# Kernel tuning notes

Measured on AMD Instinct MI355X. Metric: run time of the kernel, lower is better.

Reference implementation:

```python
import jax, jax.numpy as jnp
import numpy as np

NUM_TOKENS = 50000
TOKEN_DIM = 1024
HIDDEN = 2048
NUM_LABEL = 50000
T = 512
MAX_LEN = 50  # length-classifier has 50 classes -> max decode steps


def setup_inputs() -> dict:
    key = jax.random.key(0)
    ks = jax.random.split(key, 20)
    s = 0.02
    def nrm(k, shape):
        return jax.random.normal(k, shape, dtype=jnp.float32) * s
    return {
        "x": jax.random.randint(ks[0], (T,), 0, NUM_TOKENS),
        "E": nrm(ks[1], (NUM_TOKENS, TOKEN_DIM)),
        "L": nrm(ks[2], (NUM_LABEL, HIDDEN)),
        # forward encoder GRU (torch layout: W_ih [3H, in], W_hh [3H, H])
        "Wih_f": nrm(ks[3], (3 * HIDDEN, TOKEN_DIM)),
        "Whh_f": nrm(ks[4], (3 * HIDDEN, HIDDEN)),
        "bih_f": nrm(ks[5], (3 * HIDDEN,)),
        "bhh_f": nrm(ks[6], (3 * HIDDEN,)),
        # backward encoder GRU
        "Wih_b": nrm(ks[7], (3 * HIDDEN, TOKEN_DIM)),
        "Whh_b": nrm(ks[8], (3 * HIDDEN, HIDDEN)),
        "bih_b": nrm(ks[9], (3 * HIDDEN,)),
        "bhh_b": nrm(ks[10], (3 * HIDDEN,)),
        # middle / length linears
        "W_mid": nrm(ks[11], (HIDDEN, 2 * HIDDEN)),
        "b_mid": nrm(ks[12], (HIDDEN,)),
        "W_len": nrm(ks[13], (MAX_LEN, HIDDEN)),
        "b_len": nrm(ks[14], (MAX_LEN,)),
        # decoder GRU (input size 2H)
        "Wih_d": nrm(ks[15], (3 * HIDDEN, 2 * HIDDEN)),
        "Whh_d": nrm(ks[16], (3 * HIDDEN, HIDDEN)),
        "bih_d": nrm(ks[17], (3 * HIDDEN,)),
        "bhh_d": nrm(ks[18], (3 * HIDDEN,)),
        # final classifier (no bias)
        "W_last": nrm(ks[19], (NUM_LABEL, HIDDEN)),
    }


def _gru_final_hidden(emb, Wih, Whh, bih, bhh):
    """Run a single-layer GRU over emb [T, in] from h0=0; return final hidden [H]."""
    def step(h, x):
        gi = x @ Wih.T + bih          # [3H]
        gh = h @ Whh.T + bhh          # [3H]
        ir, iz, inn = jnp.split(gi, 3)
        hr, hz, hn = jnp.split(gh, 3)
        r = jax.nn.sigmoid(ir + hr)
        z = jax.nn.sigmoid(iz + hz)
        n = jnp.tanh(inn + r * hn)
        return (1.0 - z) * n + z * h, None
    h0 = jnp.zeros((Whh.shape[1],), emb.dtype)
    hT, _ = jax.lax.scan(step, h0, emb)
    return hT


def reference(x, E, L, Wih_f, Whh_f, bih_f, bhh_f, Wih_b, Whh_b, bih_b, bhh_b,
              W_mid, b_mid, W_len, b_len, Wih_d, Whh_d, bih_d, bhh_d, W_last):
    emb = E[x]  # [T, token_dim]
    hF = _gru_final_hidden(emb, Wih_f, Whh_f, bih_f, bhh_f)
    hB = _gru_final_hidden(emb[::-1], Wih_b, Whh_b, bih_b, bhh_b)
    sent = jnp.concatenate([hF, hB]) @ W_mid.T + b_mid   # [H]
    lscores = sent @ W_len.T + b_len                      # [50]

    # Decoder: original passes h as the GRU *input* with a fresh zero hidden
    # each step, so h-side gate preactivations reduce to bhh_d.
    hr_d, hz_d, hn_d = jnp.split(bhh_d, 3)

    def dec_step(carry, _):
        gi = carry @ Wih_d.T + bih_d          # carry: [2H]
        ir, iz, inn = jnp.split(gi, 3)
        r = jax.nn.sigmoid(ir + hr_d)
        z = jax.nn.sigmoid(iz + hz_d)
        n = jnp.tanh(inn + r * hn_d)
        h = (1.0 - z) * n                     # + z * 0 since h0 = 0
        scores = h @ W_last.T                 # [num_label]
        pred = jnp.argmax(scores)
        return jnp.concatenate([h, L[pred]]), (scores, pred)

    init = jnp.concatenate([jnp.zeros((HIDDEN,), sent.dtype), sent])
    _, (all_scores, preds) = jax.lax.scan(dec_step, init, None, length=MAX_LEN)
    # fixed MAX_LEN-step unroll; original stops at argmax(lscores) steps
    return lscores, all_scores, preds
```

## Files before the change

### kernel.cpp

```cpp
#include <hip/hip_runtime.h>
#include <math.h>

#define NWG 256
#define TPB 512
#define BSLOT 32

static constexpr int H    = 2048;
static constexpr int H3   = 6144;
static constexpr int TDIM = 1024;
static constexpr int TSEQ = 512;
static constexpr int NL   = 50000;
static constexpr int ML   = 50;
static constexpr int DK   = 4096;

static constexpr size_t OFF_EMB  = 0;
static constexpr size_t OFF_GI   = OFF_EMB + (size_t)TSEQ * TDIM * 4;
static constexpr size_t OFF_BAR  = OFF_GI + (size_t)2 * TSEQ * H3 * 4;
static constexpr size_t OFF_HBF  = OFF_BAR + (size_t)64 * BSLOT * 4;
static constexpr size_t OFF_HBB  = OFF_HBF + (size_t)2 * H * 4;
static constexpr size_t OFF_HF   = OFF_HBB + (size_t)2 * H * 4;
static constexpr size_t OFF_HB   = OFF_HF + (size_t)H * 4;
static constexpr size_t OFF_SENT = OFF_HB + (size_t)H * 4;
static constexpr size_t OFF_HD   = OFF_SENT + (size_t)H * 4;
static constexpr size_t OFF_WBV  = OFF_HD + (size_t)H * 4;
static constexpr size_t OFF_WBI  = OFF_WBV + (size_t)NWG * 4;
static constexpr size_t OFF_ONE  = OFF_WBI + (size_t)NWG * 4;
static constexpr size_t OFF_WL16 = ((OFF_ONE + 64) + 255) & ~(size_t)255;
static constexpr size_t WS_NEED  = OFF_WL16;
static constexpr size_t WS_BIG   = OFF_WL16 + (size_t)NL * H * 2;

__device__ __forceinline__ float4 cld4(const float4* p) {
  float4 v;
  asm volatile("global_load_dwordx4 %0, %1, off sc0 sc1\n\ts_waitcnt vmcnt(0)"
               : "=v"(v) : "v"(p) : "memory");
  return v;
}
__device__ __forceinline__ float cld1(const float* p) {
  float v;
  asm volatile("global_load_dword %0, %1, off sc0 sc1\n\ts_waitcnt vmcnt(0)"
               : "=v"(v) : "v"(p) : "memory");
  return v;
}
__device__ __forceinline__ int cldi(const int* p) {
  int v;
  asm volatile("global_load_dword %0, %1, off sc0 sc1\n\ts_waitcnt vmcnt(0)"
               : "=v"(v) : "v"(p) : "memory");
  return v;
}
__device__ __forceinline__ void cst1(float* p, float v) {
  asm volatile("global_store_dword %0, %1, off sc0 sc1" :: "v"(p), "v"(v) : "memory");
}
__device__ __forceinline__ void csti(int* p, int v) {
  asm volatile("global_store_dword %0, %1, off sc0 sc1" :: "v"(p), "v"(v) : "memory");
}

__device__ __forceinline__ float dp4(float4 a, float4 b, float s) {
  s = fmaf(a.x, b.x, s);
  s = fmaf(a.y, b.y, s);
  s = fmaf(a.z, b.z, s);
  s = fmaf(a.w, b.w, s);
  return s;
}
__device__ __forceinline__ float wred(float s) {
  #pragma unroll
  for (int m = 32; m > 0; m >>= 1) s += __shfl_xor(s, m, 64);
  return s;
}
__device__ __forceinline__ float u2lo(unsigned u) { return __uint_as_float(u << 16); }
__device__ __forceinline__ float u2hi(unsigned u) { return __uint_as_float(u & 0xffff0000u); }

#define DECL8(p)  float4 p##0, p##1, p##2, p##3, p##4, p##5, p##6, p##7
#define LOAD8(p, base) do { const float4* _r = (base); \
  p##0 = _r[lane];       p##1 = _r[lane + 64];  p##2 = _r[lane + 128]; \
  p##3 = _r[lane + 192]; p##4 = _r[lane + 256]; p##5 = _r[lane + 320]; \
  p##6 = _r[lane + 384]; p##7 = _r[lane + 448]; } while (0)
#define SC4(v) do { (v).x *= one; (v).y *= one; (v).z *= one; (v).w *= one; } while (0)
#define SCALE8(p) do { SC4(p##0); SC4(p##1); SC4(p##2); SC4(p##3); \
                       SC4(p##4); SC4(p##5); SC4(p##6); SC4(p##7); } while (0)
#define STEPK(k) { float4 hv = h4[lane + (k << 6)]; \
  a0r = dp4(wA##k, hv, a0r); \
  a0z = dp4(wB##k, hv, a0z); \
  a0n = dp4(wC##k, hv, a0n); \
  a1r = dp4(lwW[((k) << 6) + lane], hv, a1r); \
  a1z = dp4(lwW[(((k) + 8) << 6) + lane], hv, a1z); \
  a1n = dp4(rN1[lane + ((k) << 6)], hv, a1n); }

__device__ __forceinline__ void hbar(unsigned* bar, int gslot, int tslot,
                                     unsigned phase, unsigned grpSize, unsigned nGrp) {
  __syncthreads();
  if (threadIdx.x == 0) {
    unsigned a = __hip_atomic_fetch_add(bar + (size_t)gslot * BSLOT, 1u,
                                        __ATOMIC_RELAXED, __HIP_MEMORY_SCOPE_AGENT);
    if (a == phase * grpSize - 1u)
      __hip_atomic_fetch_add(bar + (size_t)tslot * BSLOT, 1u,
                             __ATOMIC_RELAXED, __HIP_MEMORY_SCOPE_AGENT);
    unsigned c;
    do {
      __builtin_amdgcn_s_sleep(1);
      c = __hip_atomic_load(bar + (size_t)tslot * BSLOT,
                            __ATOMIC_RELAXED, __HIP_MEMORY_SCOPE_AGENT);
    } while (c < phase * nGrp);
    asm volatile("" ::: "memory");
  }
  __syncthreads();
}

__global__ __launch_bounds__(256) void k_gather(const int* __restrict__ x,
                                                const float* __restrict__ E,
                                                float* __restrict__ emb,
                                                unsigned* __restrict__ bar,
                                                float* __restrict__ onep) {
  if (blockIdx.x == 0) {
    for (int i = threadIdx.x; i < 64 * BSLOT; i += 256) bar[i] = 0u;
    if (threadIdx.x == 0) *onep = 1.0f;
  }
  int t = blockIdx.x;
  const float4* src = (const float4*)(E + (size_t)x[t] * TDIM);
  float4* dst = (float4*)(emb + (size_t)t * TDIM);
  dst[threadIdx.x] = src[threadIdx.x];
}

__global__ __launch_bounds__(256) void k_cast(const float* __restrict__ W,
                                              unsigned short* __restrict__ O) {
  size_t i = (size_t)blockIdx.x * 2048 + (size_t)threadIdx.x * 8;
  float4 a = ((const float4*)(W + i))[0];
  float4 b = ((const float4*)(W + i))[1];
  #define CVT(f) ((( __float_as_uint(f) + 0x7FFFu + ((__float_as_uint(f) >> 16) & 1u)) >> 16) & 0xFFFFu)
  uint4 o;
  o.x = CVT(a.x) | (CVT(a.y) << 16);
  o.y = CVT(a.z) | (CVT(a.w) << 16);
  o.z = CVT(b.x) | (CVT(b.y) << 16);
  o.w = CVT(b.z) | (CVT(b.w) << 16);
  #undef CVT
  ((uint4*)(O + i))[0] = o;
}

__global__ __launch_bounds__(256) void k_gi(const float* __restrict__ emb,
                                            const float* __restrict__ Wf,
                                            const float* __restrict__ bf_,
                                            const float* __restrict__ Wb,
                                            const float* __restrict__ bb_,
                                            float* __restrict__ GI) {
  __shared__ float As[64][33];
  __shared__ float Bs[64][33];
  const int dir = blockIdx.z;
  const float* W  = dir ? Wb  : Wf;
  const float* bi = dir ? bb_ : bf_;
  const int t0 = blockIdx.x * 64, j0 = blockIdx.y * 64;
  const int tid = threadIdx.x;
  const int tx = tid & 15, ty = tid >> 4;
  float acc[4][4] = {};
  for (int k0 = 0; k0 < TDIM; k0 += 32) {
    #pragma unroll
    for (int i = 0; i < 8; ++i) {
      int idx = tid + (i << 8);
      int r = idx >> 5, kk = idx & 31;
      int tg = t0 + r;
      int arow = dir ? (TSEQ - 1 - tg) : tg;
      As[r][kk] = emb[(size_t)arow * TDIM + k0 + kk];
      Bs[r][kk] = W[(size_t)(j0 + r) * TDIM + k0 + kk];
    }
    __syncthreads();
    #pragma unroll
    for (int kk = 0; kk < 32; ++kk) {
      float a[4], b[4];
      #pragma unroll
      for (int i = 0; i < 4; ++i) a[i] = As[ty * 4 + i][kk];
      #pragma unroll
      for (int jj = 0; jj < 4; ++jj) b[jj] = Bs[tx * 4 + jj][kk];
      #pragma unroll
      for (int i = 0; i < 4; ++i)
        #pragma unroll
        for (int jj = 0; jj < 4; ++jj) acc[i][jj] = fmaf(a[i], b[jj], acc[i][jj]);
    }
    __syncthreads();
  }
  float* C = GI + (size_t)dir * TSEQ * H3;
  #pragma unroll
  for (int i = 0; i < 4; ++i)
    #pragma unroll
    for (int jj = 0; jj < 4; ++jj) {
      int t = t0 + ty * 4 + i, col = j0 + tx * 4 + jj;
      C[(size_t)t * H3 + col] = acc[i][jj] + bi[col];
    }
}

__global__ __launch_bounds__(TPB, 2) void k_enc(
    const float* __restrict__ Whh_f, const float* __restrict__ bhh_f,
    const float* __restrict__ Whh_b, const float* __restrict__ bhh_b,
    const float* __restrict__ GI,
    float* __restrict__ hbF, float* __restrict__ hbB,
    float* __restrict__ hF, float* __restrict__ hB,
    unsigned* __restrict__ bar, const float* __restrict__ onep) {
  __shared__ float  ldsH[H];
  __shared__ float4 ldsW[8 * 16 * 64];
  const int tid  = threadIdx.x;
  const int wg   = blockIdx.x;
  const int lane = tid & 63;
  const int w    = tid >> 6;
  const float4* h4 = (const float4*)ldsH;
  const float one = *onep;

  const int d   = wg >> 7;
  const int wid = wg & 127;
  const int j0  = (((wid << 3) | w) << 1);
  const float* Whh = d ? Whh_b : Whh_f;
  const float* bhh = d ? bhh_b : bhh_f;
  const float* GId = GI + (size_t)d * TSEQ * H3;
  float* hbufD = d ? hbB : hbF;
  float* hT    = d ? hB  : hF;
  const int gslot = d * 16 + (wid & 7), tslot = d * 16 + 8;
  unsigned ep = 0;

  DECL8(wA); DECL8(wB); DECL8(wC);
  LOAD8(wA, (const float4*)(Whh + (size_t)(0 * H + j0 + 0) * H));
  LOAD8(wB, (const float4*)(Whh + (size_t)(1 * H + j0 + 0) * H));
  LOAD8(wC, (const float4*)(Whh + (size_t)(2 * H + j0 + 0) * H));

  float4* lwW = &ldsW[(size_t)w << 10];
  {
    const float4* rR1 = (const float4*)(Whh + (size_t)(0 * H + j0 + 1) * H);
    const float4* rZ1 = (const float4*)(Whh + (size_t)(1 * H + j0 + 1) * H);
    #pragma unroll
    for (int k = 0; k < 8; ++k) lwW[(k << 6) + lane]       = rR1[lane + (k << 6)];
    #pragma unroll
    for (int k = 0; k < 8; ++k) lwW[((k + 8) << 6) + lane] = rZ1[lane + (k << 6)];
  }

  const float4* rN1 = (const float4*)(Whh + (size_t)(2 * H + j0 + 1) * H);

  float b_r = 0.f, b_z = 0.f, b_n = 0.f, g_r = 0.f, g_z = 0.f, g_n = 0.f;
  if (lane < 2) {
    b_r = bhh[j0 + lane]; b_z = bhh[H + j0 + lane]; b_n = bhh[2 * H + j0 + lane];
    g_r = GId[j0 + lane]; g_z = GId[H + j0 + lane]; g_n = GId[2 * H + j0 + lane];
  }
  if (lane < 2) {
    float r = 1.f / (1.f + expf(-(g_r + b_r)));
    float z = 1.f / (1.f + expf(-(g_z + b_z)));
    float n = tanhf(g_n + r * b_n);
    cst1(&hbufD[H + j0 + lane], (1.f - z) * n);
    const float* gp = GId + (size_t)1 * H3 + j0 + lane;
    g_r = gp[0]; g_z = gp[H]; g_n = gp[2 * H];
  }
  hbar(bar, gslot, tslot, ++ep, 16u, 8u);

  for (int t = 1; t < TSEQ; ++t) {
    SCALE8(wA); SCALE8(wB); SCALE8(wC);

    ((float4*)ldsH)[tid] = cld4((const float4*)hbufD + ((t & 1) << 9) + tid);
    __syncthreads();
    float a0r = 0.f, a0z = 0.f, a0n = 0.f, a1r = 0.f, a1z = 0.f, a1n = 0.f;
    STEPK(0) STEPK(1) STEPK(2) STEPK(3) STEPK(4) STEPK(5) STEPK(6) STEPK(7)
    a0r = wred(a0r); a0z = wred(a0z); a0n = wred(a0n);
    a1r = wred(a1r); a1z = wred(a1z); a1n = wred(a1n);
    if (lane < 2) {
      float aR = lane ? a1r : a0r;
      float aZ = lane ? a1z : a0z;
      float aN = lane ? a1n : a0n;
      float hold = ldsH[j0 + lane];
      float r = 1.f / (1.f + expf(-(g_r + b_r + aR)));
      float z = 1.f / (1.f + expf(-(g_z + b_z + aZ)));
      float n = tanhf(g_n + r * (aN + b_n));
      cst1(&hbufD[(size_t)((t + 1) & 1) * H + j0 + lane], (1.f - z) * n + z * hold);
      if (t < TSEQ - 1) {
        const float* gp = GId + (size_t)(t + 1) * H3 + j0 + lane;
        g_r = gp[0]; g_z = gp[H]; g_n = gp[2 * H];
      }
    }
    hbar(bar, gslot, tslot, ++ep, 16u, 8u);
  }
  if (wid == 0) {
    float4 hv = cld4((const float4*)hbufD + tid);
    ((float4*)hT)[tid] = hv;
  }
}

template <int BF16>
__global__ __launch_bounds__(TPB, 2) void k_dec(
    const float* __restrict__ W_mid, const float* __restrict__ b_mid,
    const float* __restrict__ W_len, const float* __restrict__ b_len,
    const float* __restrict__ Wih_d, const float* __restrict__ bih_d,
    const float* __restrict__ bhh_d,
    const float* __restrict__ W_last, const unsigned short* __restrict__ Wl16,
    const float* __restrict__ L,
    float* __restrict__ out,
    const float* __restrict__ hF, const float* __restrict__ hB,
    float* __restrict__ sent, float* __restrict__ hD,
    float* __restrict__ wbV, int* __restrict__ wbI,
    unsigned* __restrict__ bar) {
  __shared__ float ldsH[H];
  __shared__ float ldsC[2 * H];
  __shared__ float rv[NWG];
  __shared__ int   ri[NWG];
  __shared__ float tv1[8], tv2[8];
  __shared__ int   ti1[8], ti2[8];
  __shared__ float scV[2];
  __shared__ int   scI[2];

  const int tid  = threadIdx.x;
  const int wg   = blockIdx.x;
  const int lane = tid & 63;
  const int w    = tid >> 6;
  const float4* h4 = (const float4*)ldsH;
  const int jd = (wg << 3) | w;
  unsigned fp = 0;

  ((float4*)ldsC)[tid]       = ((const float4*)hF)[tid];
  ((float4*)ldsC)[TPB + tid] = ((const float4*)hB)[tid];
  __syncthreads();
  {
    const float4* wm = (const float4*)W_mid + (size_t)jd * (DK / 4);
    const float4* c4 = (const float4*)ldsC;
    float s = 0.f;
    #pragma unroll
    for (int k = 0; k < 16; ++k) {
      int c = lane + (k << 6);
      s = dp4(wm[c], c4[c], s);
    }
    s = wred(s);
    if (lane == 0) cst1(&sent[jd], s + b_mid[jd]);
  }
  hbar(bar, 32 + (wg & 7), 40, ++fp, 32u, 8u);

  ((float4*)ldsH)[tid] = cld4((const float4*)sent + tid);
  __syncthreads();

  if (jd < ML) {
    const float4* wl = (const float4*)W_len + (size_t)jd * (H / 4);
    float s = 0.f;
    #pragma unroll
    for (int k = 0; k < 8; ++k) {
      int c = lane + (k << 6);
      s = dp4(wl[c], h4[c], s);
    }
    s = wred(s);
    if (lane == 0) out[jd] = s + b_len[jd];
  }

  float cr = 0.f, cz = 0.f, cni = 0.f, cnh = 0.f;
  if (lane == 0) {
    cr  = bih_d[jd] + bhh_d[jd];
    cz  = bih_d[H + jd] + bhh_d[H + jd];
    cni = bih_d[2 * H + jd];
    cnh = bhh_d[2 * H + jd];
  }

  ((float4*)ldsC)[tid]       = make_float4(0.f, 0.f, 0.f, 0.f);
  ((float4*)ldsC)[TPB + tid] = ((const float4*)ldsH)[tid];
  __syncthreads();

  for (int st = 0; st < ML; ++st) {
    if (st > 0) {
      if (tid < NWG) { rv[tid] = cld1(wbV + tid); ri[tid] = cldi(wbI + tid); }
      __syncthreads();
      for (int off = NWG / 2; off > 0; off >>= 1) {
        if (tid < off) {
          float v2 = rv[tid + off]; int i2 = ri[tid + off];
          if (v2 > rv[tid] || (v2 == rv[tid] && i2 < ri[tid])) { rv[tid] = v2; ri[tid] = i2; }
        }
        __syncthreads();
      }
      int pred = ri[0];
      if (wg == 0 && tid == 0) out[ML + (size_t)ML * NL + (st - 1)] = (float)pred;
      ((float4*)ldsC)[tid]       = ((const float4*)ldsH)[tid];
      ((float4*)ldsC)[TPB + tid] = ((const float4*)(L + (size_t)pred * H))[tid];
      __syncthreads();
    }
    {
      const float4* c4 = (const float4*)ldsC;
      const float4* r0 = (const float4*)Wih_d + (size_t)jd * (DK / 4);
      const float4* r1 = r0 + (size_t)H * (DK / 4);
      const float4* r2 = r1 + (size_t)H * (DK / 4);
      float s0 = 0.f, s1 = 0.f, s2 = 0.f;
      #pragma unroll 4
      for (int k = 0; k < 16; ++k) {
        int c = lane + (k << 6);
        float4 cv = c4[c];
        s0 = dp4(r0[c], cv, s0);
        s1 = dp4(r1[c], cv, s1);
        s2 = dp4(r2[c], cv, s2);
      }
      s0 = wred(s0); s1 = wred(s1); s2 = wred(s2);
      if (lane == 0) {
        float r = 1.f / (1.f + expf(-(s0 + cr)));
        float z = 1.f / (1.f + expf(-(s1 + cz)));
        float n = tanhf(s2 + cni + r * cnh);
        cst1(&hD[jd], (1.f - z) * n);
      }
    }
    hbar(bar, 32 + (wg & 7), 40, ++fp, 32u, 8u);

    ((float4*)ldsH)[tid] = cld4((const float4*)hD + tid);
    __syncthreads();
    float* outs = out + ML + (size_t)st * NL;
    if (BF16) {
      float4 hvb[8];
      #pragma unroll
      for (int k = 0; k < 4; ++k) {
        int i = (lane + (k << 6)) << 1;
        hvb[2 * k]     = h4[i];
        hvb[2 * k + 1] = h4[i + 1];
      }
      float v1 = -3.4e38f, v2 = -3.4e38f;
      int   i1 = 0x7FFFFFFF, i2 = 0x7FFFFFFF;
      for (int chunk = 0; chunk < 25; ++chunk) {
        int r = (chunk << 11) + jd;
        if (r < NL) {
          const uint4* row = (const uint4*)(Wl16 + (size_t)r * H);
          float sc = 0.f;
          #pragma unroll
          for (int k = 0; k < 4; ++k) {
            uint4 u = row[lane + (k << 6)];
            float4 ha = hvb[2 * k], hb = hvb[2 * k + 1];
            sc = fmaf(u2lo(u.x), ha.x, sc); sc = fmaf(u2hi(u.x), ha.y, sc);
            sc = fmaf(u2lo(u.y), ha.z, sc); sc = fmaf(u2hi(u.y), ha.w, sc);
            sc = fmaf(u2lo(u.z), hb.x, sc); sc = fmaf(u2hi(u.z), hb.y, sc);
            sc = fmaf(u2lo(u.w), hb.z, sc); sc = fmaf(u2hi(u.w), hb.w, sc);
          }
          sc = wred(sc);
          if (lane == 0) outs[r] = sc;
          if (sc > v1 || (sc == v1 && r < i1)) { v2 = v1; i2 = i1; v1 = sc; i1 = r; }
          else if (sc > v2 || (sc == v2 && r < i2)) { v2 = sc; i2 = r; }
        }
      }
      if (lane == 0) { tv1[w] = v1; ti1[w] = i1; tv2[w] = v2; ti2[w] = i2; }
      __syncthreads();
      if (tid == 0) {
        float b1 = -3.4e38f, b2 = -3.4e38f;
        int   x1 = 0x7FFFFFFF, x2 = 0x7FFFFFFF;
        #pragma unroll
        for (int q = 0; q < 8; ++q) {
          float a1 = tv1[q]; int y1 = ti1[q];
          float a2 = tv2[q]; int y2 = ti2[q];
          if (a1 > b1 || (a1 == b1 && y1 < x1)) { b2 = b1; x2 = x1; b1 = a1; x1 = y1; }
          else if (a1 > b2 || (a1 == b2 && y1 < x2)) { b2 = a1; x2 = y1; }
          if (a2 > b1 || (a2 == b1 && y2 < x1)) { b2 = b1; x2 = x1; b1 = a2; x1 = y2; }
          else if (a2 > b2 || (a2 == b2 && y2 < x2)) { b2 = a2; x2 = y2; }
        }
        scI[0] = x1; scI[1] = x2;
      }
      __syncthreads();
      if (w < 2) {
        int c = scI[w];
        const float4* wl = (const float4*)W_last + (size_t)c * (H / 4);
        float s = 0.f;
        #pragma unroll
        for (int k = 0; k < 8; ++k) {
          int cc = lane + (k << 6);
          s = dp4(wl[cc], h4[cc], s);
        }
        s = wred(s);
        if (lane == 0) scV[w] = s;
      }
      __syncthreads();
      if (tid == 0) {
        float v = scV[0]; int i0 = scI[0];
        if (scV[1] > v || (scV[1] == v && scI[1] < i0)) { v = scV[1]; i0 = scI[1]; }
        cst1(&wbV[wg], v); csti(&wbI[wg], i0);
      }
    } else {
      float4 hv[8];
      #pragma unroll
      for (int k = 0; k < 8; ++k) hv[k] = h4[lane + (k << 6)];
      float bv = -3.4e38f; int bix = 0x7FFFFFFF;
      for (int chunk = 0; chunk < 25; ++chunk) {
        int r = (chunk << 11) + jd;
        if (r < NL) {
          const float4* wl = (const float4*)W_last + (size_t)r * (H / 4);
          float sc = 0.f;
          #pragma unroll
          for (int k = 0; k < 8; ++k) sc = dp4(wl[lane + (k << 6)], hv[k], sc);
          sc = wred(sc);
          if (lane == 0) {
            outs[r] = sc;
            if (sc > bv) { bv = sc; bix = r; }
          }
        }
      }
      if (lane == 0) { tv1[w] = bv; ti1[w] = bix; }
      __syncthreads();
      if (tid == 0) {
        float v = tv1[0]; int i0 = ti1[0];
        #pragma unroll
        for (int q = 1; q < 8; ++q)
          if (tv1[q] > v || (tv1[q] == v && ti1[q] < i0)) { v = tv1[q]; i0 = ti1[q]; }
        cst1(&wbV[wg], v); csti(&wbI[wg], i0);
      }
    }
    hbar(bar, 32 + (wg & 7), 40, ++fp, 32u, 8u);
  }

  if (wg == 0) {
    if (tid < NWG) { rv[tid] = cld1(wbV + tid); ri[tid] = cldi(wbI + tid); }
    __syncthreads();
    for (int off = NWG / 2; off > 0; off >>= 1) {
      if (tid < off) {
        float v2 = rv[tid + off]; int i2 = ri[tid + off];
        if (v2 > rv[tid] || (v2 == rv[tid] && i2 < ri[tid])) { rv[tid] = v2; ri[tid] = i2; }
      }
      __syncthreads();
    }
    if (tid == 0) out[ML + (size_t)ML * NL + (ML - 1)] = (float)ri[0];
  }
}

extern "C" void kernel_launch(void* const* d_in, const int* in_sizes, int n_in,
                              void* d_out, int out_size, void* d_ws, size_t ws_size,
                              hipStream_t stream) {
  (void)in_sizes; (void)n_in; (void)out_size;
  if (ws_size < WS_NEED) return;
  const bool big = (ws_size >= WS_BIG);

  const int*   x     = (const int*)  d_in[0];
  const float* E     = (const float*)d_in[1];
  const float* L     = (const float*)d_in[2];
  const float* Wih_f = (const float*)d_in[3];
  const float* Whh_f = (const float*)d_in[4];
  const float* bih_f = (const float*)d_in[5];
  const float* bhh_f = (const float*)d_in[6];
  const float* Wih_b = (const float*)d_in[7];
  const float* Whh_b = (const float*)d_in[8];
  const float* bih_b = (const float*)d_in[9];
  const float* bhh_b = (const float*)d_in[10];
  const float* W_mid = (const float*)d_in[11];
  const float* b_mid = (const float*)d_in[12];
  const float* W_len = (const float*)d_in[13];
  const float* b_len = (const float*)d_in[14];
  const float* Wih_d = (const float*)d_in[15];
  const float* bih_d = (const float*)d_in[17];
  const float* bhh_d = (const float*)d_in[18];
  const float* W_last= (const float*)d_in[19];
  float* out = (float*)d_out;
  char* ws = (char*)d_ws;

  float*    emb  = (float*)(ws + OFF_EMB);
  float*    GIp  = (float*)(ws + OFF_GI);
  unsigned* bar  = (unsigned*)(ws + OFF_BAR);
  float*    hbF  = (float*)(ws + OFF_HBF);
  float*    hbB  = (float*)(ws + OFF_HBB);
  float*    hF   = (float*)(ws + OFF_HF);
  float*    hB   = (float*)(ws + OFF_HB);
  float*    sent = (float*)(ws + OFF_SENT);
  float*    hD   = (float*)(ws + OFF_HD);
  float*    wbV  = (float*)(ws + OFF_WBV);
  int*      wbI  = (int*)  (ws + OFF_WBI);
  float*    onep = (float*)(ws + OFF_ONE);
  unsigned short* wl16 = (unsigned short*)(ws + OFF_WL16);

  hipLaunchKernelGGL(k_gather, dim3(TSEQ), dim3(256), 0, stream, x, E, emb, bar, onep);
  if (big)
    hipLaunchKernelGGL(k_cast, dim3(NL), dim3(256), 0, stream, W_last, wl16);
  hipLaunchKernelGGL(k_gi, dim3(TSEQ / 64, H3 / 64, 2), dim3(256), 0, stream,
                     emb, Wih_f, bih_f, Wih_b, bih_b, GIp);
  hipLaunchKernelGGL(k_enc, dim3(NWG), dim3(TPB), 0, stream,
                     Whh_f, bhh_f, Whh_b, bhh_b, GIp, hbF, hbB, hF, hB, bar, onep);
  if (big)
    hipLaunchKernelGGL(k_dec<1>, dim3(NWG), dim3(TPB), 0, stream,
                       W_mid, b_mid, W_len, b_len, Wih_d, bih_d, bhh_d,
                       W_last, wl16, L, out, hF, hB, sent, hD, wbV, wbI, bar);
  else
    hipLaunchKernelGGL(k_dec<0>, dim3(NWG), dim3(TPB), 0, stream,
                       W_mid, b_mid, W_len, b_len, Wih_d, bih_d, bhh_d,
                       W_last, wl16, L, out, hF, hB, sent, hD, wbV, wbI, bar);
}
```

Before: 5.457 ms.

## Double decoder workgroup size and split GRU matvec across half-K waves

The decoder kernel now runs 1024 threads (16 waves) per workgroup instead of 512. The decoder GRU and W_mid matvecs split each output row's K range across two waves and combine the partial sums through shared memory. The W_last scoring loop spreads rows over twice as many waves, with fewer chunks per wave. The aim is more loads in flight per CU for the bandwidth-bound decoder, at the cost of an extra LDS reduction and sync and a tighter per-thread register budget from the new launch bounds.

```diff
diff --git a/kernel.cpp b/kernel.cpp
--- a/kernel.cpp
+++ b/kernel.cpp
@@ -3,6 +3,7 @@
 
 #define NWG 256
 #define TPB 512
+#define TPBD 1024
 #define BSLOT 32
 
 static constexpr int H    = 2048;
@@ -276,7 +277,7 @@
 }
 
 template <int BF16>
-__global__ __launch_bounds__(TPB, 2) void k_dec(
+__global__ __launch_bounds__(TPBD, 4) void k_dec(
     const float* __restrict__ W_mid, const float* __restrict__ b_mid,
     const float* __restrict__ W_len, const float* __restrict__ b_len,
     const float* __restrict__ Wih_d, const float* __restrict__ bih_d,
@@ -292,8 +293,9 @@
   __shared__ float ldsC[2 * H];
   __shared__ float rv[NWG];
   __shared__ int   ri[NWG];
-  __shared__ float tv1[8], tv2[8];
-  __shared__ int   ti1[8], ti2[8];
+  __shared__ float tv1[16], tv2[16];
+  __shared__ int   ti1[16], ti2[16];
+  __shared__ float pS0[16], pS1[16], pS2[16];
   __shared__ float scV[2];
   __shared__ int   scI[2];
 
@@ -301,32 +303,36 @@
   const int wg   = blockIdx.x;
   const int lane = tid & 63;
   const int w    = tid >> 6;
+  const int gw   = (wg << 4) | w;
+  const int jdA  = (wg << 3) | (w & 7);
+  const int kb   = (w >> 3) << 3;
   const float4* h4 = (const float4*)ldsH;
-  const int jd = (wg << 3) | w;
   unsigned fp = 0;
 
-  ((float4*)ldsC)[tid]       = ((const float4*)hF)[tid];
-  ((float4*)ldsC)[TPB + tid] = ((const float4*)hB)[tid];
+  ((float4*)ldsC)[tid] = (tid < 512) ? ((const float4*)hF)[tid]
+                                     : ((const float4*)hB)[tid - 512];
   __syncthreads();
   {
-    const float4* wm = (const float4*)W_mid + (size_t)jd * (DK / 4);
+    const float4* wm = (const float4*)W_mid + (size_t)jdA * (DK / 4);
     const float4* c4 = (const float4*)ldsC;
     float s = 0.f;
     #pragma unroll
-    for (int k = 0; k < 16; ++k) {
-      int c = lane + (k << 6);
+    for (int k = 0; k < 8; ++k) {
+      int c = lane + ((k + kb) << 6);
       s = dp4(wm[c], c4[c], s);
     }
     s = wred(s);
-    if (lane == 0) cst1(&sent[jd], s + b_mid[jd]);
-  }
+    if (lane == 0) pS0[w] = s;
+  }
+  __syncthreads();
+  if (w < 8 && lane == 0) cst1(&sent[jdA], pS0[w] + pS0[w + 8] + b_mid[jdA]);
   hbar(bar, 32 + (wg & 7), 40, ++fp, 32u, 8u);
 
-  ((float4*)ldsH)[tid] = cld4((const float4*)sent + tid);
+  if (tid < 512) ((float4*)ldsH)[tid] = cld4((const float4*)sent + tid);
   __syncthreads();
 
-  if (jd < ML) {
-    const float4* wl = (const float4*)W_len + (size_t)jd * (H / 4);
+  if (gw < ML) {
+    const float4* wl = (const float4*)W_len + (size_t)gw * (H / 4);
     float s = 0.f;
     #pragma unroll
     for (int k = 0; k < 8; ++k) {
@@ -334,19 +340,19 @@
       s = dp4(wl[c], h4[c], s);
     }
     s = wred(s);
-    if (lane == 0) out[jd] = s + b_len[jd];
+    if (lane == 0) out[gw] = s + b_len[gw];
   }
 
   float cr = 0.f, cz = 0.f, cni = 0.f, cnh = 0.f;
-  if (lane == 0) {
-    cr  = bih_d[jd] + bhh_d[jd];
-    cz  = bih_d[H + jd] + bhh_d[H + jd];
-    cni = bih_d[2 * H + jd];
-    cnh = bhh_d[2 * H + jd];
-  }
-
-  ((float4*)ldsC)[tid]       = make_float4(0.f, 0.f, 0.f, 0.f);
-  ((float4*)ldsC)[TPB + tid] = ((const float4*)ldsH)[tid];
+  if (w < 8 && lane == 0) {
+    cr  = bih_d[jdA] + bhh_d[jdA];
+    cz  = bih_d[H + jdA] + bhh_d[H + jdA];
+    cni = bih_d[2 * H + jdA];
+    cnh = bhh_d[2 * H + jdA];
+  }
+
+  ((float4*)ldsC)[tid] = (tid < 512) ? make_float4(0.f, 0.f, 0.f, 0.f)
+                                     : ((const float4*)ldsH)[tid - 512];
   __syncthreads();
 
   for (int st = 0; st < ML; ++st) {
@@ -362,35 +368,41 @@
       }
       int pred = ri[0];
       if (wg == 0 && tid == 0) out[ML + (size_t)ML * NL + (st - 1)] = (float)pred;
-      ((float4*)ldsC)[tid]       = ((const float4*)ldsH)[tid];
-      ((float4*)ldsC)[TPB + tid] = ((const float4*)(L + (size_t)pred * H))[tid];
+      ((float4*)ldsC)[tid] = (tid < 512)
+          ? ((const float4*)ldsH)[tid]
+          : ((const float4*)(L + (size_t)pred * H))[tid - 512];
       __syncthreads();
     }
     {
       const float4* c4 = (const float4*)ldsC;
-      const float4* r0 = (const float4*)Wih_d + (size_t)jd * (DK / 4);
+      const float4* r0 = (const float4*)Wih_d + (size_t)jdA * (DK / 4);
       const float4* r1 = r0 + (size_t)H * (DK / 4);
       const float4* r2 = r1 + (size_t)H * (DK / 4);
       float s0 = 0.f, s1 = 0.f, s2 = 0.f;
-      #pragma unroll 4
-      for (int k = 0; k < 16; ++k) {
-        int c = lane + (k << 6);
+      #pragma unroll
+      for (int k = 0; k < 8; ++k) {
+        int c = lane + ((k + kb) << 6);
         float4 cv = c4[c];
         s0 = dp4(r0[c], cv, s0);
         s1 = dp4(r1[c], cv, s1);
         s2 = dp4(r2[c], cv, s2);
       }
       s0 = wred(s0); s1 = wred(s1); s2 = wred(s2);
-      if (lane == 0) {
-        float r = 1.f / (1.f + expf(-(s0 + cr)));
-        float z = 1.f / (1.f + expf(-(s1 + cz)));
-        float n = tanhf(s2 + cni + r * cnh);
-        cst1(&hD[jd], (1.f - z) * n);
+      if (lane == 0) { pS0[w] = s0; pS1[w] = s1; pS2[w] = s2; }
+      __syncthreads();
+      if (w < 8 && lane == 0) {
+        float t0 = pS0[w] + pS0[w + 8];
+        float t1 = pS1[w] + pS1[w + 8];
+        float t2 = pS2[w] + pS2[w + 8];
+        float r = 1.f / (1.f + expf(-(t0 + cr)));
+        float z = 1.f / (1.f + expf(-(t1 + cz)));
+        float n = tanhf(t2 + cni + r * cnh);
+        cst1(&hD[jdA], (1.f - z) * n);
       }
     }
     hbar(bar, 32 + (wg & 7), 40, ++fp, 32u, 8u);
 
-    ((float4*)ldsH)[tid] = cld4((const float4*)hD + tid);
+    if (tid < 512) ((float4*)ldsH)[tid] = cld4((const float4*)hD + tid);
     __syncthreads();
     float* outs = out + ML + (size_t)st * NL;
     if (BF16) {
@@ -403,8 +415,8 @@
       }
       float v1 = -3.4e38f, v2 = -3.4e38f;
       int   i1 = 0x7FFFFFFF, i2 = 0x7FFFFFFF;
-      for (int chunk = 0; chunk < 25; ++chunk) {
-        int r = (chunk << 11) + jd;
+      for (int chunk = 0; chunk < 13; ++chunk) {
+        int r = (chunk << 12) + gw;
         if (r < NL) {
           const uint4* row = (const uint4*)(Wl16 + (size_t)r * H);
           float sc = 0.f;
@@ -429,7 +441,7 @@
         float b1 = -3.4e38f, b2 = -3.4e38f;
         int   x1 = 0x7FFFFFFF, x2 = 0x7FFFFFFF;
         #pragma unroll
-        for (int q = 0; q < 8; ++q) {
+        for (int q = 0; q < 16; ++q) {
           float a1 = tv1[q]; int y1 = ti1[q];
           float a2 = tv2[q]; int y2 = ti2[q];
           if (a1 > b1 || (a1 == b1 && y1 < x1)) { b2 = b1; x2 = x1; b1 = a1; x1 = y1; }
@@ -463,8 +475,8 @@
       #pragma unroll
       for (int k = 0; k < 8; ++k) hv[k] = h4[lane + (k << 6)];
       float bv = -3.4e38f; int bix = 0x7FFFFFFF;
-      for (int chunk = 0; chunk < 25; ++chunk) {
-        int r = (chunk << 11) + jd;
+      for (int chunk = 0; chunk < 13; ++chunk) {
+        int r = (chunk << 12) + gw;
         if (r < NL) {
           const float4* wl = (const float4*)W_last + (size_t)r * (H / 4);
           float sc = 0.f;
@@ -482,7 +494,7 @@
       if (tid == 0) {
         float v = tv1[0]; int i0 = ti1[0];
         #pragma unroll
-        for (int q = 1; q < 8; ++q)
+        for (int q = 1; q < 16; ++q)
           if (tv1[q] > v || (tv1[q] == v && ti1[q] < i0)) { v = tv1[q]; i0 = ti1[q]; }
         cst1(&wbV[wg], v); csti(&wbI[wg], i0);
       }
@@ -555,11 +567,11 @@
   hipLaunchKernelGGL(k_enc, dim3(NWG), dim3(TPB), 0, stream,
                      Whh_f, bhh_f, Whh_b, bhh_b, GIp, hbF, hbB, hF, hB, bar, onep);
   if (big)
-    hipLaunchKernelGGL(k_dec<1>, dim3(NWG), dim3(TPB), 0, stream,
+    hipLaunchKernelGGL(k_dec<1>, dim3(NWG), dim3(TPBD), 0, stream,
                        W_mid, b_mid, W_len, b_len, Wih_d, bih_d, bhh_d,
                        W_last, wl16, L, out, hF, hB, sent, hD, wbV, wbI, bar);
   else
-    hipLaunchKernelGGL(k_dec<0>, dim3(NWG), dim3(TPB), 0, stream,
+    hipLaunchKernelGGL(k_dec<0>, dim3(NWG), dim3(TPBD), 0, stream,
                        W_mid, b_mid, W_len, b_len, Wih_d, bih_d, bhh_d,
                        W_last, wl16, L, out, hF, hB, sent, hD, wbV, wbI, bar);
 }
```

New measurement: 6.376 ms. 16.8% more time.

## Keep decoder input-gate weights resident in registers and LDS across decode steps

Applied to the files above, without the earlier changes.

Each workgroup's slice of Wih_d (3 rows × 4096 per wave) is loaded once before the decode loop. Part of it is held in registers (scaled by a runtime 'one' so the compiler cannot rematerialize the loads), part goes into 128KB of LDS, and the rest is still streamed from global memory. This avoids rereading about 100MB of Wih_d on each of the 50 steps. The classifier loops now read h straight from LDS instead of preloading it into registers, and the bf16 score stores become nontemporal. The cost is much higher register and LDS pressure, which may lower occupancy or cause spills; launch_bounds(512,2) cannot be met with 128KB+ of LDS per block.

```diff
diff --git a/kernel.cpp b/kernel.cpp
--- a/kernel.cpp
+++ b/kernel.cpp
@@ -12,6 +12,8 @@
 static constexpr int NL   = 50000;
 static constexpr int ML   = 50;
 static constexpr int DK   = 4096;
+
+typedef unsigned int v4u __attribute__((ext_vector_type(4)));
 
 static constexpr size_t OFF_EMB  = 0;
 static constexpr size_t OFF_GI   = OFF_EMB + (size_t)TSEQ * TDIM * 4;
@@ -84,6 +86,14 @@
   a1r = dp4(lwW[((k) << 6) + lane], hv, a1r); \
   a1z = dp4(lwW[(((k) + 8) << 6) + lane], hv, a1z); \
   a1n = dp4(rN1[lane + ((k) << 6)], hv, a1n); }
+#define DSTEPA(k) { float4 cv = c4[lane + ((k) << 6)]; \
+  s0 = dp4(wRa##k, cv, s0); \
+  s1 = dp4(wZa##k, cv, s1); \
+  s2 = dp4(lwW[512 + ((k) << 6) + lane], cv, s2); }
+#define DSTEPB(j) { float4 cv = c4[lane + (((j) + 8) << 6)]; \
+  s0 = dp4(wRb##j, cv, s0); \
+  s1 = dp4(lwW[((j) << 6) + lane], cv, s1); \
+  s2 = dp4(rN2[lane + ((j) << 6)], cv, s2); }
 
 __device__ __forceinline__ void hbar(unsigned* bar, int gslot, int tslot,
                                      unsigned phase, unsigned grpSize, unsigned nGrp) {
@@ -287,9 +297,10 @@
     const float* __restrict__ hF, const float* __restrict__ hB,
     float* __restrict__ sent, float* __restrict__ hD,
     float* __restrict__ wbV, int* __restrict__ wbI,
-    unsigned* __restrict__ bar) {
-  __shared__ float ldsH[H];
-  __shared__ float ldsC[2 * H];
+    unsigned* __restrict__ bar, const float* __restrict__ onep) {
+  __shared__ float  ldsH[H];
+  __shared__ float  ldsC[2 * H];
+  __shared__ float4 ldsW[8 * 1024];
   __shared__ float rv[NWG];
   __shared__ int   ri[NWG];
   __shared__ float tv1[8], tv2[8];
@@ -303,7 +314,24 @@
   const int w    = tid >> 6;
   const float4* h4 = (const float4*)ldsH;
   const int jd = (wg << 3) | w;
+  const float one = *onep;
   unsigned fp = 0;
+
+  const float4* rowR = (const float4*)Wih_d + (size_t)jd * (DK / 4);
+  const float4* rowZ = rowR + (size_t)H * (DK / 4);
+  const float4* rowN = rowZ + (size_t)H * (DK / 4);
+  DECL8(wRa); DECL8(wRb); DECL8(wZa);
+  LOAD8(wRa, rowR);
+  LOAD8(wRb, rowR + 512);
+  LOAD8(wZa, rowZ);
+  float4* lwW = &ldsW[(size_t)w << 10];
+  {
+    #pragma unroll
+    for (int k = 0; k < 8; ++k) lwW[(k << 6) + lane]       = rowZ[512 + (k << 6) + lane];
+    #pragma unroll
+    for (int k = 0; k < 8; ++k) lwW[512 + (k << 6) + lane] = rowN[(k << 6) + lane];
+  }
+  const float4* rN2 = rowN + 512;
 
   ((float4*)ldsC)[tid]       = ((const float4*)hF)[tid];
   ((float4*)ldsC)[TPB + tid] = ((const float4*)hB)[tid];
@@ -367,19 +395,13 @@
       __syncthreads();
     }
     {
+      SCALE8(wRa); SCALE8(wRb); SCALE8(wZa);
       const float4* c4 = (const float4*)ldsC;
-      const float4* r0 = (const float4*)Wih_d + (size_t)jd * (DK / 4);
-      const float4* r1 = r0 + (size_t)H * (DK / 4);
-      const float4* r2 = r1 + (size_t)H * (DK / 4);
       float s0 = 0.f, s1 = 0.f, s2 = 0.f;
-      #pragma unroll 4
-      for (int k = 0; k < 16; ++k) {
-        int c = lane + (k << 6);
-        float4 cv = c4[c];
-        s0 = dp4(r0[c], cv, s0);
-        s1 = dp4(r1[c], cv, s1);
-        s2 = dp4(r2[c], cv, s2);
-      }
+      DSTEPA(0) DSTEPA(1) DSTEPA(2) DSTEPA(3)
+      DSTEPA(4) DSTEPA(5) DSTEPA(6) DSTEPA(7)
+      DSTEPB(0) DSTEPB(1) DSTEPB(2) DSTEPB(3)
+      DSTEPB(4) DSTEPB(5) DSTEPB(6) DSTEPB(7)
       s0 = wred(s0); s1 = wred(s1); s2 = wred(s2);
       if (lane == 0) {
         float r = 1.f / (1.f + expf(-(s0 + cr)));
@@ -394,13 +416,6 @@
     __syncthreads();
     float* outs = out + ML + (size_t)st * NL;
     if (BF16) {
-      float4 hvb[8];
-      #pragma unroll
-      for (int k = 0; k < 4; ++k) {
-        int i = (lane + (k << 6)) << 1;
-        hvb[2 * k]     = h4[i];
-        hvb[2 * k + 1] = h4[i + 1];
-      }
       float v1 = -3.4e38f, v2 = -3.4e38f;
       int   i1 = 0x7FFFFFFF, i2 = 0x7FFFFFFF;
       for (int chunk = 0; chunk < 25; ++chunk) {
@@ -411,14 +426,15 @@
           #pragma unroll
           for (int k = 0; k < 4; ++k) {
             uint4 u = row[lane + (k << 6)];
-            float4 ha = hvb[2 * k], hb = hvb[2 * k + 1];
+            int i = (lane + (k << 6)) << 1;
+            float4 ha = h4[i], hb = h4[i + 1];
             sc = fmaf(u2lo(u.x), ha.x, sc); sc = fmaf(u2hi(u.x), ha.y, sc);
             sc = fmaf(u2lo(u.y), ha.z, sc); sc = fmaf(u2hi(u.y), ha.w, sc);
             sc = fmaf(u2lo(u.z), hb.x, sc); sc = fmaf(u2hi(u.z), hb.y, sc);
             sc = fmaf(u2lo(u.w), hb.z, sc); sc = fmaf(u2hi(u.w), hb.w, sc);
           }
           sc = wred(sc);
-          if (lane == 0) outs[r] = sc;
+          if (lane == 0) __builtin_nontemporal_store(sc, &outs[r]);
           if (sc > v1 || (sc == v1 && r < i1)) { v2 = v1; i2 = i1; v1 = sc; i1 = r; }
           else if (sc > v2 || (sc == v2 && r < i2)) { v2 = sc; i2 = r; }
         }
@@ -459,9 +475,6 @@
         cst1(&wbV[wg], v); csti(&wbI[wg], i0);
       }
     } else {
-      float4 hv[8];
-      #pragma unroll
-      for (int k = 0; k < 8; ++k) hv[k] = h4[lane + (k << 6)];
       float bv = -3.4e38f; int bix = 0x7FFFFFFF;
       for (int chunk = 0; chunk < 25; ++chunk) {
         int r = (chunk << 11) + jd;
@@ -469,7 +482,10 @@
           const float4* wl = (const float4*)W_last + (size_t)r * (H / 4);
           float sc = 0.f;
           #pragma unroll
-          for (int k = 0; k < 8; ++k) sc = dp4(wl[lane + (k << 6)], hv[k], sc);
+          for (int k = 0; k < 8; ++k) {
+            int c = lane + (k << 6);
+            sc = dp4(wl[c], h4[c], sc);
+          }
           sc = wred(sc);
           if (lane == 0) {
             outs[r] = sc;
@@ -557,9 +573,9 @@
   if (big)
     hipLaunchKernelGGL(k_dec<1>, dim3(NWG), dim3(TPB), 0, stream,
                        W_mid, b_mid, W_len, b_len, Wih_d, bih_d, bhh_d,
-                       W_last, wl16, L, out, hF, hB, sent, hD, wbV, wbI, bar);
+                       W_last, wl16, L, out, hF, hB, sent, hD, wbV, wbI, bar, onep);
   else
     hipLaunchKernelGGL(k_dec<0>, dim3(NWG), dim3(TPB), 0, stream,
                        W_mid, b_mid, W_len, b_len, Wih_d, bih_d, bhh_d,
-                       W_last, wl16, L, out, hF, hB, sent, hD, wbV, wbI, bar);
-}
+                       W_last, wl16, L, out, hF, hB, sent, hD, wbV, wbI, bar, onep);
+}
```

Result: no change. 5.545 ms (+1.6%).
